# Kernel tuning notes

Measured on AMD Instinct MI355X. Metric: run time of the kernel, lower is better.

The kernel has to match this reference:

```python
import jax, jax.numpy as jnp
import numpy as np
from jax import lax

N_EXPERTS = 256
N_GROUP = 8
TOPK_GROUP = 4
TOP_K = 8
AUX_ALPHA = 0.001


def setup_inputs() -> dict:
    key = jax.random.key(0)
    k1, k2 = jax.random.split(key)
    hidden_states = jax.random.normal(k1, (16384, 2048), dtype=jnp.float32)
    weight = jax.random.normal(k2, (N_EXPERTS, 2048), dtype=jnp.float32) * 0.02
    return {"hidden_states": hidden_states, "weight": weight}


def reference(hidden_states, weight):
    n_tokens = hidden_states.shape[0]
    group_size = N_EXPERTS // N_GROUP  # 32

    # gating logits: [N, E]
    logits = jnp.einsum('nh,eh->ne', hidden_states, weight)

    # group-restricted top-k: [N, G, group_size] -> top TOPK_GROUP per group
    group_logits = logits.reshape(n_tokens, N_GROUP, group_size)
    gw, gi = lax.top_k(group_logits, TOPK_GROUP)          # [N, G, tg]
    gw = gw.reshape(n_tokens, N_GROUP * TOPK_GROUP)
    gi = gi.reshape(n_tokens, N_GROUP * TOPK_GROUP)

    # global top-k over the pooled group winners
    topk_weights, ti = lax.top_k(gw, TOP_K)               # [N, K]
    selected_group = ti // TOPK_GROUP
    expert_in_group = jnp.take_along_axis(gi, ti, axis=1)
    topk_idx = selected_group * group_size + expert_in_group  # [N, K]

    # norm_topk_prob=True
    topk_weights = topk_weights / (jnp.sum(topk_weights, axis=-1, keepdims=True) + 1e-20)

    # auxiliary load-balancing loss (training path)
    expert_mask = jax.nn.one_hot(topk_idx.reshape(-1), N_EXPERTS, dtype=jnp.float32)
    expert_counts = expert_mask.mean(axis=0)              # [E]
    expert_probs = jax.nn.softmax(logits, axis=-1).mean(axis=0)  # [E]
    aux_loss = jnp.sum(expert_counts * expert_probs) * AUX_ALPHA

    return topk_idx, topk_weights, aux_loss
```

## Files before the change

kernel.cpp:

```cpp
#include <hip/hip_runtime.h>
#include <math.h>

#define NTOK 16384
#define KD   2048
#define NE   256
#define BM   32
#define NSTEP 64
#define EPS  2.5e-4f

using bf16x8 = __attribute__((ext_vector_type(8))) short;
using f32x16 = __attribute__((ext_vector_type(16))) float;
using u16 = unsigned short;
using u32 = unsigned int;

__device__ __forceinline__ u16 f2bf(float x) {
    u32 u = __float_as_uint(x);
    return (u16)((u + 0x7FFFu + ((u >> 16) & 1u)) >> 16);
}
__device__ __forceinline__ float bf2f(u16 h) {
    return __uint_as_float(((u32)h) << 16);
}

__global__ __launch_bounds__(256) void wsplit_kernel(
    const float* __restrict__ wgt, u16* __restrict__ Whi, u16* __restrict__ Wlo)
{
    const int idx = blockIdx.x * 256 + threadIdx.x;
    const int e  = idx >> 8;
    const int ko = idx & 255;
    const int k  = ko * 8;
    const int c  = k >> 5, s = (k >> 4) & 1, kh = (k >> 3) & 1;
    const int dst = (c * 2 + s) * 4096 + (e >> 6) * 1024 + ((e >> 5) & 1) * 512
                  + kh * 256 + (e & 31) * 8;
    const float* p = wgt + (size_t)e * KD + k;
    u16 hi[8], lo[8];
#pragma unroll
    for (int i = 0; i < 8; ++i) {
        const float w = p[i];
        hi[i] = f2bf(w);
        lo[i] = f2bf(w - bf2f(hi[i]));
    }
    *(uint4*)(Whi + dst) = *(const uint4*)hi;
    *(uint4*)(Wlo + dst) = *(const uint4*)lo;
}

typedef __attribute__((address_space(1))) const void GV;
typedef __attribute__((address_space(3))) void LV;
__device__ __forceinline__ void gld_lds16(const void* g, void* l) {
    __builtin_amdgcn_global_load_lds((GV*)g, (LV*)l, 16, 0, 0);
}

#define MFMA32(A, B, C) __builtin_amdgcn_mfma_f32_32x32x16_bf16((A), (B), (C), 0, 0, 0)

__global__ __launch_bounds__(256) void gate_kernel(
    const float* __restrict__ hid, const u16* __restrict__ Whi, const u16* __restrict__ Wlo,
    float* __restrict__ out, float* __restrict__ cnt, float* __restrict__ prb,
    int* __restrict__ flagcnt, int* __restrict__ flaglist)
{
    __shared__ union {
        struct { u16 bh[2][8192]; u16 bl[2][8192]; } st;
        float ls[BM][257];
    } sh;
    __shared__ u16 ah[2][BM][40], al[2][BM][40];
    __shared__ float maxS[BM], sumS[BM], invS[BM];

    const int tid  = threadIdx.x;
    const int lane = tid & 63;
    const int wv   = tid >> 6;
    const int ln31 = lane & 31;
    const int kh8  = (lane >> 5) * 8;
    const int t0   = blockIdx.x * BM;

    f32x16 acc[2];
#pragma unroll
    for (int nf = 0; nf < 2; ++nf)
#pragma unroll
        for (int r = 0; r < 16; ++r) acc[nf][r] = 0.f;

    float4 areg;
    const int am = tid >> 3;
    const int ak = (tid & 7) * 4;

    auto loadA = [&](int c) {
        areg = *(const float4*)(hid + (size_t)(t0 + am) * KD + c * 32 + ak);
    };
    auto writeA = [&](int buf) {
        float f[4] = {areg.x, areg.y, areg.z, areg.w};
#pragma unroll
        for (int i = 0; i < 4; ++i) {
            const u16 hi = f2bf(f[i]);
            ah[buf][am][ak + i] = hi;
            al[buf][am][ak + i] = f2bf(f[i] - bf2f(hi));
        }
    };
    auto stageB = [&](int c, int buf) {
        const u16* srch = Whi + (size_t)c * 8192 + tid * 8;
        const u16* srcl = Wlo + (size_t)c * 8192 + tid * 8;
        u16* dsth = &sh.st.bh[buf][tid * 8];
        u16* dstl = &sh.st.bl[buf][tid * 8];
#pragma unroll
        for (int seg = 0; seg < 4; ++seg) {
            gld_lds16(srch + seg * 2048, dsth + seg * 2048);
            gld_lds16(srcl + seg * 2048, dstl + seg * 2048);
        }
    };

    loadA(0); stageB(0, 0); writeA(0);
    int cur = 0;

#pragma unroll 1
    for (int c = 0; c < NSTEP; ++c) {
        __syncthreads();
        const int nxt = cur ^ 1;
        if (c + 1 < NSTEP) { loadA(c + 1); stageB(c + 1, nxt); }

#pragma unroll
        for (int s = 0; s < 2; ++s) {
            const int boff = s * 4096 + wv * 1024 + lane * 8;
            const bf16x8 bh0 = *(const bf16x8*)&sh.st.bh[cur][boff];
            const bf16x8 bl0 = *(const bf16x8*)&sh.st.bl[cur][boff];
            const bf16x8 bh1 = *(const bf16x8*)&sh.st.bh[cur][boff + 512];
            const bf16x8 bl1 = *(const bf16x8*)&sh.st.bl[cur][boff + 512];
            const bf16x8 a_h = *(const bf16x8*)&ah[cur][ln31][s * 16 + kh8];
            const bf16x8 a_l = *(const bf16x8*)&al[cur][ln31][s * 16 + kh8];

            acc[0] = MFMA32(a_h, bh0, acc[0]);
            acc[0] = MFMA32(a_h, bl0, acc[0]);
            acc[0] = MFMA32(a_l, bh0, acc[0]);
            acc[1] = MFMA32(a_h, bh1, acc[1]);
            acc[1] = MFMA32(a_h, bl1, acc[1]);
            acc[1] = MFMA32(a_l, bh1, acc[1]);
        }
        if (c + 1 < NSTEP) writeA(nxt);
        cur = nxt;
    }

    __syncthreads();
#pragma unroll
    for (int nf = 0; nf < 2; ++nf) {
        const int col = wv * 64 + nf * 32 + ln31;
#pragma unroll
        for (int r = 0; r < 16; ++r) {
            const int row = (r & 3) + 8 * (r >> 2) + 4 * (lane >> 5);
            sh.ls[row][col] = acc[nf][r];
        }
    }
    if (tid < BM) sumS[tid] = 0.f;
    __syncthreads();

    if (tid < BM) {
        const float* lr = &sh.ls[tid][0];
        float tv[9]; int ti[9];
#pragma unroll
        for (int j = 0; j < 9; ++j) { tv[j] = -1e30f; ti[j] = 0; }
        float gv3[8], gv4[8];
        float rowmax = -1e30f;

        auto ins9 = [&](float v, int idx) {
#pragma unroll
            for (int p = 0; p < 9; ++p) {
                if (v > tv[p]) {
#pragma unroll
                    for (int q = 8; q > p; --q) { tv[q] = tv[q - 1]; ti[q] = ti[q - 1]; }
                    tv[p] = v; ti[p] = idx;
                    break;
                }
            }
        };

#pragma unroll 1
        for (int g = 0; g < 8; ++g) {
            float v0 = -1e30f, v1 = -1e30f, v2 = -1e30f, v3 = -1e30f, v4 = -1e30f;
            int   i0 = 0, i1 = 0, i2 = 0, i3 = 0;
            for (int j = 0; j < 32; ++j) {
                const float v = lr[g * 32 + j];
                if (v > v0)      { v4=v3; v3=v2;i3=i2; v2=v1;i2=i1; v1=v0;i1=i0; v0=v;i0=j; }
                else if (v > v1) { v4=v3; v3=v2;i3=i2; v2=v1;i2=i1; v1=v;i1=j; }
                else if (v > v2) { v4=v3; v3=v2;i3=i2; v2=v;i2=j; }
                else if (v > v3) { v4=v3; v3=v;i3=j; }
                else if (v > v4) { v4=v; }
            }
            rowmax = fmaxf(rowmax, v0);
            gv3[g] = v3; gv4[g] = v4;
            ins9(v0, g * 32 + i0);
            ins9(v1, g * 32 + i1);
            ins9(v2, g * 32 + i2);
            ins9(v3, g * 32 + i3);
        }

        bool flag = false;
#pragma unroll
        for (int r = 0; r < 8; ++r)
            if (tv[r] - tv[r + 1] < EPS) flag = true;
#pragma unroll
        for (int g = 0; g < 8; ++g)
            if (gv3[g] - gv4[g] < EPS && gv3[g] > tv[7] - EPS) flag = true;

        const float s01 = __fadd_rn(tv[0], tv[1]);
        const float s23 = __fadd_rn(tv[2], tv[3]);
        const float s45 = __fadd_rn(tv[4], tv[5]);
        const float s67 = __fadd_rn(tv[6], tv[7]);
        float s = __fadd_rn(__fadd_rn(s01, s23), __fadd_rn(s45, s67));
        s = __fadd_rn(s, 1e-20f);

        const size_t tg2 = (size_t)(t0 + tid);
#pragma unroll
        for (int j = 0; j < 8; ++j) {
            out[tg2 * 8 + j]                    = (float)ti[j];
            out[(size_t)NTOK * 8 + tg2 * 8 + j] = __fdiv_rn(tv[j], s);
            atomicAdd(&cnt[ti[j]], 1.0f);
        }
        if (flag) {
            const int fi = atomicAdd(flagcnt, 1);
            flaglist[fi] = t0 + tid;
        }
        maxS[tid] = rowmax;
    }
    __syncthreads();

    {
        const int t  = tid >> 3;
        const int c0 = (tid & 7) * 32;
        const float m = maxS[t];
        float part = 0.f;
#pragma unroll
        for (int j = 0; j < 32; ++j) part += __expf(sh.ls[t][c0 + j] - m);
        atomicAdd(&sumS[t], part);
    }
    __syncthreads();
    if (tid < BM) invS[tid] = 1.0f / sumS[tid];
    __syncthreads();

    {
        float p = 0.f;
#pragma unroll
        for (int n = 0; n < BM; ++n) p += __expf(sh.ls[n][tid] - maxS[n]) * invS[n];
        atomicAdd(&prb[tid], p);
    }
}

__global__ __launch_bounds__(256) void exact_kernel(
    const float* __restrict__ hid, const float* __restrict__ wgt,
    float* __restrict__ out, float* __restrict__ cnt,
    const int* __restrict__ flagcnt, const int* __restrict__ flaglist)
{
    const int fn = *flagcnt;

    __shared__ float wch[256 * 17];
    __shared__ float hch[8 * 17];
    __shared__ float exls[8][257];
    __shared__ int tk[8];

    const int tid = threadIdx.x;
    const int tg  = tid >> 7;
    const int eg  = (tid >> 2) & 31;
    const int l   = tid & 3;

#pragma unroll 1
    for (int base = blockIdx.x * 8; base < fn; base += gridDim.x * 8) {
        const int nt = min(8, fn - base);
        __syncthreads();
        if (tid < 8) tk[tid] = (tid < nt) ? flaglist[base + tid] : flaglist[base];
        __syncthreads();

        float accq[4][8];
#pragma unroll
        for (int i = 0; i < 4; ++i)
#pragma unroll
            for (int j = 0; j < 8; ++j) accq[i][j] = 0.f;

#pragma unroll 1
        for (int c = 0; c < 128; ++c) {
            __syncthreads();
            {
                const float* p = wgt + (size_t)tid * KD + c * 16;
                float4 w0 = *(const float4*)(p);
                float4 w1 = *(const float4*)(p + 4);
                float4 w2 = *(const float4*)(p + 8);
                float4 w3 = *(const float4*)(p + 12);
                float* wr = &wch[tid * 17];
                wr[0]=w0.x; wr[1]=w0.y; wr[2]=w0.z; wr[3]=w0.w;
                wr[4]=w1.x; wr[5]=w1.y; wr[6]=w1.z; wr[7]=w1.w;
                wr[8]=w2.x; wr[9]=w2.y; wr[10]=w2.z; wr[11]=w2.w;
                wr[12]=w3.x; wr[13]=w3.y; wr[14]=w3.z; wr[15]=w3.w;
            }
            if (tid < 128) {
                const int tok = tid >> 4, k = tid & 15;
                hch[tok * 17 + k] = hid[(size_t)tk[tok] * KD + c * 16 + k];
            }
            __syncthreads();

#pragma unroll
            for (int q = 3; q >= 0; --q) {
                const int k = 4 * q + l;
                float hv[4], wv2[8];
#pragma unroll
                for (int i = 0; i < 4; ++i) hv[i] = hch[(tg * 4 + i) * 17 + k];
#pragma unroll
                for (int j = 0; j < 8; ++j) wv2[j] = wch[(j * 32 + eg) * 17 + k];
#pragma unroll
                for (int i = 0; i < 4; ++i)
#pragma unroll
                    for (int j = 0; j < 8; ++j)
                        accq[i][j] = __fadd_rn(__fmul_rn(hv[i], wv2[j]), accq[i][j]);
            }
        }

        __syncthreads();
#pragma unroll
        for (int i = 0; i < 4; ++i)
#pragma unroll
            for (int j = 0; j < 8; ++j) {
                float v = accq[i][j];
                v = __fadd_rn(v, __shfl_xor(v, 1));
                v = __fadd_rn(v, __shfl_xor(v, 2));
                if (l == 0) exls[tg * 4 + i][j * 32 + eg] = v;
            }
        __syncthreads();

        if (tid < nt) {
            const float* lr = &exls[tid][0];
            float tv[8]; int ti[8];
#pragma unroll
            for (int j = 0; j < 8; ++j) { tv[j] = -1e30f; ti[j] = 0; }

            auto ins8 = [&](float v, int idx) {
#pragma unroll
                for (int p = 0; p < 8; ++p) {
                    if (v > tv[p]) {
#pragma unroll
                        for (int q = 7; q > p; --q) { tv[q] = tv[q - 1]; ti[q] = ti[q - 1]; }
                        tv[p] = v; ti[p] = idx;
                        break;
                    }
                }
            };

#pragma unroll 1
            for (int g = 0; g < 8; ++g) {
                float v0 = -1e30f, v1 = -1e30f, v2 = -1e30f, v3 = -1e30f;
                int   i0 = 0, i1 = 0, i2 = 0, i3 = 0;
                for (int j = 0; j < 32; ++j) {
                    const float v = lr[g * 32 + j];
                    if (v > v0)      { v3=v2;i3=i2; v2=v1;i2=i1; v1=v0;i1=i0; v0=v;i0=j; }
                    else if (v > v1) { v3=v2;i3=i2; v2=v1;i2=i1; v1=v;i1=j; }
                    else if (v > v2) { v3=v2;i3=i2; v2=v;i2=j; }
                    else if (v > v3) { v3=v;i3=j; }
                }
                ins8(v0, g * 32 + i0);
                ins8(v1, g * 32 + i1);
                ins8(v2, g * 32 + i2);
                ins8(v3, g * 32 + i3);
            }

            const float s01 = __fadd_rn(tv[0], tv[1]);
            const float s23 = __fadd_rn(tv[2], tv[3]);
            const float s45 = __fadd_rn(tv[4], tv[5]);
            const float s67 = __fadd_rn(tv[6], tv[7]);
            float s = __fadd_rn(__fadd_rn(s01, s23), __fadd_rn(s45, s67));
            s = __fadd_rn(s, 1e-20f);

            const size_t gt = (size_t)tk[tid];
#pragma unroll
            for (int j = 0; j < 8; ++j) {
                const int oldi = (int)out[gt * 8 + j];
                if (oldi != ti[j]) {
                    atomicAdd(&cnt[oldi], -1.0f);
                    atomicAdd(&cnt[ti[j]], 1.0f);
                }
                out[gt * 8 + j]                    = (float)ti[j];
                out[(size_t)NTOK * 8 + gt * 8 + j] = __fdiv_rn(tv[j], s);
            }
        }
        __syncthreads();
    }
}

__global__ void aux_kernel(const float* __restrict__ cnt,
                           const float* __restrict__ prb,
                           float* __restrict__ out)
{
    const int tid = threadIdx.x;
    float v = cnt[tid] * prb[tid];
#pragma unroll
    for (int off = 32; off; off >>= 1) v += __shfl_down(v, off, 64);
    __shared__ float ps[4];
    if ((tid & 63) == 0) ps[tid >> 6] = v;
    __syncthreads();
    if (tid == 0) {
        const float tot = ps[0] + ps[1] + ps[2] + ps[3];
        out[(size_t)NTOK * 8 * 2] = tot * (0.001f / (131072.0f * 16384.0f));
    }
}

extern "C" void kernel_launch(void* const* d_in, const int* in_sizes, int n_in,
                              void* d_out, int out_size, void* d_ws, size_t ws_size,
                              hipStream_t stream)
{
    (void)in_sizes; (void)n_in; (void)out_size; (void)ws_size;
    const float* hid = (const float*)d_in[0];
    const float* wgt = (const float*)d_in[1];
    float* out = (float*)d_out;

    float* cnt      = (float*)d_ws;
    float* prb      = cnt + NE;
    int*   flagcnt  = (int*)(prb + NE);
    int*   flaglist = flagcnt + 64;
    u16*   Whi      = (u16*)(flaglist + NTOK);
    u16*   Wlo      = Whi + (size_t)NE * KD;

    hipMemsetAsync(d_ws, 0, (2 * NE + 64) * sizeof(float), stream);
    wsplit_kernel<<<NE * KD / 8 / 256, 256, 0, stream>>>(wgt, Whi, Wlo);
    gate_kernel<<<NTOK / BM, 256, 0, stream>>>(hid, Whi, Wlo, out, cnt, prb, flagcnt, flaglist);
    exact_kernel<<<256, 256, 0, stream>>>(hid, wgt, out, cnt, flagcnt, flaglist);
    aux_kernel<<<1, 256, 0, stream>>>(cnt, prb, out);
}
```

Baseline: 516.5 us.

## Enlarge gate tile to 128 tokens with 8 waves, widen exact kernel batch

The gate GEMM block grows from 32 to 128 tokens and from 256 to 512 threads. Each wave now owns 32 experts across four 32-row M-fragments, so every B fragment read from LDS feeds four MFMA groups, and the weight split layout is reordered to match. The A staging buffers move into the shared union. The exact fallback kernel now processes 32 flagged tokens per block with 1024 threads. The cost is that only 128 gate blocks launch, which is fewer than the CU count, and each block needs a large LDS footprint that limits occupancy.

```diff
diff --git a/kernel.cpp b/kernel.cpp
--- a/kernel.cpp
+++ b/kernel.cpp
@@ -4,7 +4,7 @@
 #define NTOK 16384
 #define KD   2048
 #define NE   256
-#define BM   32
+#define BM   128
 #define NSTEP 64
 #define EPS  2.5e-4f
 
@@ -29,8 +29,7 @@
     const int ko = idx & 255;
     const int k  = ko * 8;
     const int c  = k >> 5, s = (k >> 4) & 1, kh = (k >> 3) & 1;
-    const int dst = (c * 2 + s) * 4096 + (e >> 6) * 1024 + ((e >> 5) & 1) * 512
-                  + kh * 256 + (e & 31) * 8;
+    const int dst = (c * 2 + s) * 4096 + (e >> 5) * 512 + kh * 256 + (e & 31) * 8;
     const float* p = wgt + (size_t)e * KD + k;
     u16 hi[8], lo[8];
 #pragma unroll
@@ -51,16 +50,20 @@
 
 #define MFMA32(A, B, C) __builtin_amdgcn_mfma_f32_32x32x16_bf16((A), (B), (C), 0, 0, 0)
 
-__global__ __launch_bounds__(256) void gate_kernel(
+__global__ __launch_bounds__(512) void gate_kernel(
     const float* __restrict__ hid, const u16* __restrict__ Whi, const u16* __restrict__ Wlo,
     float* __restrict__ out, float* __restrict__ cnt, float* __restrict__ prb,
     int* __restrict__ flagcnt, int* __restrict__ flaglist)
 {
     __shared__ union {
-        struct { u16 bh[2][8192]; u16 bl[2][8192]; } st;
+        struct {
+            u16 bh[2][8192];
+            u16 bl[2][8192];
+            u16 ah[2][BM][40];
+            u16 al[2][BM][40];
+        } st;
         float ls[BM][257];
     } sh;
-    __shared__ u16 ah[2][BM][40], al[2][BM][40];
     __shared__ float maxS[BM], sumS[BM], invS[BM];
 
     const int tid  = threadIdx.x;
@@ -70,26 +73,28 @@
     const int kh8  = (lane >> 5) * 8;
     const int t0   = blockIdx.x * BM;
 
-    f32x16 acc[2];
-#pragma unroll
-    for (int nf = 0; nf < 2; ++nf)
-#pragma unroll
-        for (int r = 0; r < 16; ++r) acc[nf][r] = 0.f;
-
-    float4 areg;
-    const int am = tid >> 3;
-    const int ak = (tid & 7) * 4;
+    f32x16 acc[4];
+#pragma unroll
+    for (int mf = 0; mf < 4; ++mf)
+#pragma unroll
+        for (int r = 0; r < 16; ++r) acc[mf][r] = 0.f;
+
+    float4 arg0, arg1;
+    const int am = tid >> 2;
+    const int ak = (tid & 3) * 8;
 
     auto loadA = [&](int c) {
-        areg = *(const float4*)(hid + (size_t)(t0 + am) * KD + c * 32 + ak);
+        const float* p = hid + (size_t)(t0 + am) * KD + c * 32 + ak;
+        arg0 = *(const float4*)p;
+        arg1 = *(const float4*)(p + 4);
     };
     auto writeA = [&](int buf) {
-        float f[4] = {areg.x, areg.y, areg.z, areg.w};
-#pragma unroll
-        for (int i = 0; i < 4; ++i) {
+        float f[8] = {arg0.x, arg0.y, arg0.z, arg0.w, arg1.x, arg1.y, arg1.z, arg1.w};
+#pragma unroll
+        for (int i = 0; i < 8; ++i) {
             const u16 hi = f2bf(f[i]);
-            ah[buf][am][ak + i] = hi;
-            al[buf][am][ak + i] = f2bf(f[i] - bf2f(hi));
+            sh.st.ah[buf][am][ak + i] = hi;
+            sh.st.al[buf][am][ak + i] = f2bf(f[i] - bf2f(hi));
         }
     };
     auto stageB = [&](int c, int buf) {
@@ -97,11 +102,10 @@
         const u16* srcl = Wlo + (size_t)c * 8192 + tid * 8;
         u16* dsth = &sh.st.bh[buf][tid * 8];
         u16* dstl = &sh.st.bl[buf][tid * 8];
-#pragma unroll
-        for (int seg = 0; seg < 4; ++seg) {
-            gld_lds16(srch + seg * 2048, dsth + seg * 2048);
-            gld_lds16(srcl + seg * 2048, dstl + seg * 2048);
-        }
+        gld_lds16(srch,        dsth);
+        gld_lds16(srch + 4096, dsth + 4096);
+        gld_lds16(srcl,        dstl);
+        gld_lds16(srcl + 4096, dstl + 4096);
     };
 
     loadA(0); stageB(0, 0); writeA(0);
@@ -115,20 +119,17 @@
 
 #pragma unroll
         for (int s = 0; s < 2; ++s) {
-            const int boff = s * 4096 + wv * 1024 + lane * 8;
-            const bf16x8 bh0 = *(const bf16x8*)&sh.st.bh[cur][boff];
-            const bf16x8 bl0 = *(const bf16x8*)&sh.st.bl[cur][boff];
-            const bf16x8 bh1 = *(const bf16x8*)&sh.st.bh[cur][boff + 512];
-            const bf16x8 bl1 = *(const bf16x8*)&sh.st.bl[cur][boff + 512];
-            const bf16x8 a_h = *(const bf16x8*)&ah[cur][ln31][s * 16 + kh8];
-            const bf16x8 a_l = *(const bf16x8*)&al[cur][ln31][s * 16 + kh8];
-
-            acc[0] = MFMA32(a_h, bh0, acc[0]);
-            acc[0] = MFMA32(a_h, bl0, acc[0]);
-            acc[0] = MFMA32(a_l, bh0, acc[0]);
-            acc[1] = MFMA32(a_h, bh1, acc[1]);
-            acc[1] = MFMA32(a_h, bl1, acc[1]);
-            acc[1] = MFMA32(a_l, bh1, acc[1]);
+            const int bo = s * 4096 + wv * 512 + (lane >> 5) * 256 + ln31 * 8;
+            const bf16x8 bh = *(const bf16x8*)&sh.st.bh[cur][bo];
+            const bf16x8 bl = *(const bf16x8*)&sh.st.bl[cur][bo];
+#pragma unroll
+            for (int mf = 0; mf < 4; ++mf) {
+                const bf16x8 a_h = *(const bf16x8*)&sh.st.ah[cur][mf * 32 + ln31][s * 16 + kh8];
+                const bf16x8 a_l = *(const bf16x8*)&sh.st.al[cur][mf * 32 + ln31][s * 16 + kh8];
+                acc[mf] = MFMA32(a_h, bh, acc[mf]);
+                acc[mf] = MFMA32(a_h, bl, acc[mf]);
+                acc[mf] = MFMA32(a_l, bh, acc[mf]);
+            }
         }
         if (c + 1 < NSTEP) writeA(nxt);
         cur = nxt;
@@ -136,12 +137,12 @@
 
     __syncthreads();
 #pragma unroll
-    for (int nf = 0; nf < 2; ++nf) {
-        const int col = wv * 64 + nf * 32 + ln31;
+    for (int mf = 0; mf < 4; ++mf) {
+        const int col = wv * 32 + ln31;
 #pragma unroll
         for (int r = 0; r < 16; ++r) {
-            const int row = (r & 3) + 8 * (r >> 2) + 4 * (lane >> 5);
-            sh.ls[row][col] = acc[nf][r];
+            const int row = mf * 32 + (r & 3) + 8 * (r >> 2) + 4 * (lane >> 5);
+            sh.ls[row][col] = acc[mf][r];
         }
     }
     if (tid < BM) sumS[tid] = 0.f;
@@ -218,27 +219,27 @@
     __syncthreads();
 
     {
-        const int t  = tid >> 3;
-        const int c0 = (tid & 7) * 32;
+        const int t  = tid >> 2;
+        const int c0 = (tid & 3) * 64;
         const float m = maxS[t];
         float part = 0.f;
 #pragma unroll
-        for (int j = 0; j < 32; ++j) part += __expf(sh.ls[t][c0 + j] - m);
+        for (int j = 0; j < 64; ++j) part += __expf(sh.ls[t][c0 + j] - m);
         atomicAdd(&sumS[t], part);
     }
     __syncthreads();
     if (tid < BM) invS[tid] = 1.0f / sumS[tid];
     __syncthreads();
 
-    {
+    if (tid < NE) {
         float p = 0.f;
-#pragma unroll
+#pragma unroll 4
         for (int n = 0; n < BM; ++n) p += __expf(sh.ls[n][tid] - maxS[n]) * invS[n];
         atomicAdd(&prb[tid], p);
     }
 }
 
-__global__ __launch_bounds__(256) void exact_kernel(
+__global__ __launch_bounds__(1024) void exact_kernel(
     const float* __restrict__ hid, const float* __restrict__ wgt,
     float* __restrict__ out, float* __restrict__ cnt,
     const int* __restrict__ flagcnt, const int* __restrict__ flaglist)
@@ -246,9 +247,9 @@
     const int fn = *flagcnt;
 
     __shared__ float wch[256 * 17];
-    __shared__ float hch[8 * 17];
-    __shared__ float exls[8][257];
-    __shared__ int tk[8];
+    __shared__ float hch[32 * 17];
+    __shared__ float exls[32][257];
+    __shared__ int tk[32];
 
     const int tid = threadIdx.x;
     const int tg  = tid >> 7;
@@ -256,10 +257,10 @@
     const int l   = tid & 3;
 
 #pragma unroll 1
-    for (int base = blockIdx.x * 8; base < fn; base += gridDim.x * 8) {
-        const int nt = min(8, fn - base);
-        __syncthreads();
-        if (tid < 8) tk[tid] = (tid < nt) ? flaglist[base + tid] : flaglist[base];
+    for (int base = blockIdx.x * 32; base < fn; base += gridDim.x * 32) {
+        const int nt = min(32, fn - base);
+        __syncthreads();
+        if (tid < 32) tk[tid] = (tid < nt) ? flaglist[base + tid] : flaglist[base];
         __syncthreads();
 
         float accq[4][8];
@@ -272,18 +273,13 @@
         for (int c = 0; c < 128; ++c) {
             __syncthreads();
             {
-                const float* p = wgt + (size_t)tid * KD + c * 16;
-                float4 w0 = *(const float4*)(p);
-                float4 w1 = *(const float4*)(p + 4);
-                float4 w2 = *(const float4*)(p + 8);
-                float4 w3 = *(const float4*)(p + 12);
-                float* wr = &wch[tid * 17];
-                wr[0]=w0.x; wr[1]=w0.y; wr[2]=w0.z; wr[3]=w0.w;
-                wr[4]=w1.x; wr[5]=w1.y; wr[6]=w1.z; wr[7]=w1.w;
-                wr[8]=w2.x; wr[9]=w2.y; wr[10]=w2.z; wr[11]=w2.w;
-                wr[12]=w3.x; wr[13]=w3.y; wr[14]=w3.z; wr[15]=w3.w;
-            }
-            if (tid < 128) {
+                const int e  = tid >> 2;
+                const int q4 = (tid & 3) * 4;
+                const float4 w = *(const float4*)(wgt + (size_t)e * KD + c * 16 + q4);
+                float* wr = &wch[e * 17 + q4];
+                wr[0] = w.x; wr[1] = w.y; wr[2] = w.z; wr[3] = w.w;
+            }
+            if (tid < 512) {
                 const int tok = tid >> 4, k = tid & 15;
                 hch[tok * 17 + k] = hid[(size_t)tk[tok] * KD + c * 16 + k];
             }
@@ -410,7 +406,7 @@
 
     hipMemsetAsync(d_ws, 0, (2 * NE + 64) * sizeof(float), stream);
     wsplit_kernel<<<NE * KD / 8 / 256, 256, 0, stream>>>(wgt, Whi, Wlo);
-    gate_kernel<<<NTOK / BM, 256, 0, stream>>>(hid, Whi, Wlo, out, cnt, prb, flagcnt, flaglist);
-    exact_kernel<<<256, 256, 0, stream>>>(hid, wgt, out, cnt, flagcnt, flaglist);
+    gate_kernel<<<NTOK / BM, 512, 0, stream>>>(hid, Whi, Wlo, out, cnt, prb, flagcnt, flaglist);
+    exact_kernel<<<128, 1024, 0, stream>>>(hid, wgt, out, cnt, flagcnt, flaglist);
     aux_kernel<<<1, 256, 0, stream>>>(cnt, prb, out);
 }
```

After: 676.8 us. 31.0% more time.
